# Kernel tuning notes

Hardware: AMD Instinct MI355X
Metric: run time of the kernel (lower is better)

The kernel has to match this reference:

```python
import jax, jax.numpy as jnp
import numpy as np

N_NODES = 50000


def _sage_layer(x, edges, W_neigh, W_self, b):
    """HeteroGraphConv(sum) of per-relation DGL SAGEConv(mean).

    x:        [N, F_in] node features (single node type)
    edges:    [R, 2, E] int (src, dst) per relation
    W_neigh:  [R, F_in, F_out], W_self: [R, F_in, F_out], b: [R, F_out]
    returns:  [N, F_out]
    """
    N = x.shape[0]
    R = edges.shape[0]
    out = jnp.zeros((N, W_neigh.shape[-1]), dtype=x.dtype)
    for r in range(R):  # small fixed number of relation types
        src = edges[r, 0]
        dst = edges[r, 1]
        # mean-aggregate neighbor features onto dst
        s = jax.ops.segment_sum(x[src], dst, num_segments=N)          # [N, F_in]
        deg = jax.ops.segment_sum(jnp.ones_like(dst, dtype=x.dtype), dst,
                                  num_segments=N)                     # [N]
        mean = s / jnp.maximum(deg, 1.0)[:, None]                     # zero-deg -> 0
        # SAGEConv(mean): fc_self(h_dst) + fc_neigh(mean_neigh) + bias
        out = out + x @ W_self[r] + mean @ W_neigh[r] + b[r]
    return out


def setup_inputs() -> dict:
    key = jax.random.key(0)
    ks = jax.random.split(key, 10)
    F_in, H, O, R, E = 128, 128, 64, 2, 800000
    scale_in = 1.0 / np.sqrt(F_in)
    scale_h = 1.0 / np.sqrt(H)
    return {
        "x": jax.random.normal(ks[0], (N_NODES, F_in), dtype=jnp.float32),
        "edges": jax.random.randint(ks[1], (R, 2, E), 0, N_NODES, dtype=jnp.int32),
        "neg_edges": jax.random.randint(ks[2], (2, E), 0, N_NODES, dtype=jnp.int32),
        "W_neigh1": jax.random.normal(ks[3], (R, F_in, H), jnp.float32) * scale_in,
        "W_self1": jax.random.normal(ks[4], (R, F_in, H), jnp.float32) * scale_in,
        "b1": jnp.zeros((R, H), jnp.float32),
        "W_neigh2": jax.random.normal(ks[5], (R, H, O), jnp.float32) * scale_h,
        "W_self2": jax.random.normal(ks[6], (R, H, O), jnp.float32) * scale_h,
        "b2": jnp.zeros((R, O), jnp.float32),
    }


def reference(x, edges, neg_edges, W_neigh1, W_self1, b1, W_neigh2, W_self2, b2):
    h = _sage_layer(x, edges, W_neigh1, W_self1, b1)
    h = jax.nn.relu(h)
    h = _sage_layer(h, edges, W_neigh2, W_self2, b2)          # [N, O]
    # HeteroDotProductPredictor: u_dot_v on edges of the scored etype (rel 0)
    pos_score = jnp.sum(h[edges[0, 0]] * h[edges[0, 1]], axis=-1)      # [E]
    neg_score = jnp.sum(h[neg_edges[0]] * h[neg_edges[1]], axis=-1)    # [E_neg]
    return pos_score, neg_score
```

## Files before the change

kernel.cpp:

```cpp
#include <hip/hip_runtime.h>


#define BW 128
#define NBK_MAX 1024
#define EPB 8192

typedef __attribute__((ext_vector_type(8))) short bf16x8;
typedef __attribute__((ext_vector_type(4))) float floatx4;
typedef __attribute__((ext_vector_type(2))) float floatx2;

__device__ __forceinline__ unsigned short f2bf(float f) {
    unsigned u = __float_as_uint(f);
    unsigned r = u + 0x7FFFu + ((u >> 16) & 1u);
    return (unsigned short)(r >> 16);
}
__device__ __forceinline__ unsigned pack2(float a, float b) {
    return (unsigned)f2bf(a) | ((unsigned)f2bf(b) << 16);
}
__device__ __forceinline__ float bflo(unsigned v) { return __uint_as_float(v << 16); }
__device__ __forceinline__ float bfhi(unsigned v) { return __uint_as_float(v & 0xFFFF0000u); }
#define RFL(x) __builtin_amdgcn_readfirstlane(x)

#if defined(__has_builtin) && __has_builtin(__builtin_amdgcn_cvt_pk_f32_fp8)
__device__ __forceinline__ floatx2 fp8lo(unsigned v) {
    return __builtin_amdgcn_cvt_pk_f32_fp8((int)v, false);
}
__device__ __forceinline__ floatx2 fp8hi(unsigned v) {
    return __builtin_amdgcn_cvt_pk_f32_fp8((int)v, true);
}
#else
__device__ __forceinline__ float fp8_1(unsigned b) {
    return __uint_as_float(((b & 0x80u) << 24) | ((b & 0x7Fu) << 20)) * 0x1.0p+120f;
}
__device__ __forceinline__ floatx2 fp8lo(unsigned v) {
    floatx2 r; r.x = fp8_1(v & 0xFFu); r.y = fp8_1((v >> 8) & 0xFFu); return r;
}
__device__ __forceinline__ floatx2 fp8hi(unsigned v) {
    floatx2 r; r.x = fp8_1((v >> 16) & 0xFFu); r.y = fp8_1((v >> 24) & 0xFFu); return r;
}
#endif

#if defined(__has_builtin) && __has_builtin(__builtin_amdgcn_cvt_pk_fp8_f32)
__device__ __forceinline__ unsigned f32x4_fp8x4(float a, float b, float c, float d) {
    unsigned lo = __builtin_amdgcn_cvt_pk_fp8_f32(a, b, 0, false);
    return __builtin_amdgcn_cvt_pk_fp8_f32(c, d, lo, true);
}
#else
__device__ __forceinline__ unsigned f2fp8(float x) {
    float m = fminf(fabsf(x), 448.0f);
    unsigned u = __float_as_uint(m * 0x1.0p-120f);
    unsigned r = (u + 0x7FFFFu + ((u >> 20) & 1u)) >> 20;
    if (r > 0x7Eu) r = 0x7Eu;
    return r | ((__float_as_uint(x) >> 24) & 0x80u);
}
__device__ __forceinline__ unsigned f32x4_fp8x4(float a, float b, float c, float d) {
    return f2fp8(a) | (f2fp8(b) << 8) | (f2fp8(c) << 16) | (f2fp8(d) << 24);
}
#endif

__global__ __launch_bounds__(256) void
bucket_count_kernel(const int* __restrict__ edges, int* __restrict__ bcnt,
                    int NBK, int E)
{
    __shared__ int cnt[2 * NBK_MAX];
    const int rbT = 2 * NBK;
    const int t = threadIdx.x;
    for (int k = t; k < rbT; k += 256) cnt[k] = 0;
    __syncthreads();
    long long start = (long long)blockIdx.x * EPB;
    long long twoE = 2LL * E;
    for (int u = 0; u < EPB / 256; ++u) {
        long long idx = start + u * 256 + t;
        if (idx < twoE) {
            int r = idx >= E;
            int e = (int)(idx - (long long)r * E);
            int d = edges[(size_t)r * 2 * E + E + e];
            atomicAdd(&cnt[r * NBK + (d >> 7)], 1);
        }
    }
    __syncthreads();
    for (int k = t; k < rbT; k += 256)
        if (cnt[k]) atomicAdd(&bcnt[k], cnt[k]);
}

__global__ __launch_bounds__(1024) void
bucket_scan_kernel(const int* __restrict__ bcnt, int* __restrict__ bko,
                   int rbT, int twoE)
{
    __shared__ int sm[1024];
    int t = threadIdx.x;
    int v = (t < rbT) ? bcnt[t] : 0;
    sm[t] = v;
    __syncthreads();
    for (int s = 1; s < 1024; s <<= 1) {
        int u = (t >= s) ? sm[t - s] : 0;
        __syncthreads();
        sm[t] += u;
        __syncthreads();
    }
    if (t < rbT) bko[t] = sm[t] - v;
    if (t == 0) bko[rbT] = twoE;
}

__global__ __launch_bounds__(256) void
partition_kernel(const int* __restrict__ edges, const int* __restrict__ bko,
                 int* __restrict__ gcur, uint2* __restrict__ staging,
                 int NBK, int E)
{
    __shared__ int cnt[2 * NBK_MAX];
    __shared__ int base[2 * NBK_MAX];
    const int rbT = 2 * NBK;
    const int t = threadIdx.x;
    for (int k = t; k < rbT; k += 256) cnt[k] = 0;
    __syncthreads();
    long long start = (long long)blockIdx.x * EPB;
    long long twoE = 2LL * E;
    for (int u = 0; u < EPB / 256; ++u) {
        long long idx = start + u * 256 + t;
        if (idx < twoE) {
            int r = idx >= E;
            int e = (int)(idx - (long long)r * E);
            int d = edges[(size_t)r * 2 * E + E + e];
            atomicAdd(&cnt[r * NBK + (d >> 7)], 1);
        }
    }
    __syncthreads();
    for (int k = t; k < rbT; k += 256) {
        int c0 = cnt[k];
        if (c0) base[k] = bko[k] + atomicAdd(&gcur[k], c0);
        cnt[k] = 0;
    }
    __syncthreads();
    for (int u = 0; u < EPB / 256; ++u) {
        long long idx = start + u * 256 + t;
        if (idx < twoE) {
            int r = idx >= E;
            int e = (int)(idx - (long long)r * E);
            int s = edges[(size_t)r * 2 * E + e];
            int d = edges[(size_t)r * 2 * E + E + e];
            int rb = r * NBK + (d >> 7);
            int pos = atomicAdd(&cnt[rb], 1);
            staging[(size_t)base[rb] + pos] = make_uint2((unsigned)s, (unsigned)d);
        }
    }
}

__global__ __launch_bounds__(256) void
bucket_csr_kernel(const uint2* __restrict__ staging, const int* __restrict__ bko,
                  int* __restrict__ csr, int* __restrict__ off,
                  int NBK, int N)
{
    __shared__ int hist[BW], excl[BW], cur[BW], sc[BW];
    const int rb = blockIdx.x;
    const int r = rb / NBK;
    const int b = rb % NBK;
    const int node0 = b * BW;
    const int nn = min(BW, N - node0);
    const int cbase = bko[rb];
    const int c = bko[rb + 1] - cbase;
    const int t = threadIdx.x;

    if (t < BW) { hist[t] = 0; cur[t] = 0; }
    __syncthreads();
    for (int k = t; k < c; k += 256)
        atomicAdd(&hist[(int)staging[(size_t)cbase + k].y - node0], 1);
    __syncthreads();
    if (t < BW) sc[t] = hist[t];
    __syncthreads();
    for (int s = 1; s < BW; s <<= 1) {
        int v = (t < BW && t >= s) ? sc[t - s] : 0;
        __syncthreads();
        if (t < BW) sc[t] += v;
        __syncthreads();
    }
    if (t < BW) excl[t] = sc[t] - hist[t];
    if (t < nn) off[(size_t)r * N + node0 + t] = cbase + excl[t];
    __syncthreads();
    for (int k = t; k < c; k += 256) {
        uint2 pr = staging[(size_t)cbase + k];
        int l = (int)pr.y - node0;
        int pos = atomicAdd(&cur[l], 1);
        csr[(size_t)cbase + excl[l] + pos] = (int)pr.x;
    }
}

__global__ void cvt_kernel(const float* __restrict__ in,
                           unsigned short* __restrict__ o,
                           unsigned char* __restrict__ o8, int n4)
{
    int t = blockIdx.x * blockDim.x + threadIdx.x;
    if (t >= n4) return;
    float4 v = ((const float4*)in)[t];
    ushort4 r;
    r.x = f2bf(v.x); r.y = f2bf(v.y); r.z = f2bf(v.z); r.w = f2bf(v.w);
    ((ushort4*)o)[t] = r;
    ((unsigned*)o8)[t] = f32x4_fp8x4(v.x, v.y, v.z, v.w);
}

__global__ void prep_kernel(const float* __restrict__ Ws1, const float* __restrict__ Wn1,
                            const float* __restrict__ b1,
                            const float* __restrict__ Ws2, const float* __restrict__ Wn2,
                            const float* __restrict__ b2,
                            unsigned short* __restrict__ WT1z, unsigned short* __restrict__ WT1a,
                            unsigned short* __restrict__ WT1b, float* __restrict__ bc1,
                            unsigned short* __restrict__ WT2z, unsigned short* __restrict__ WT2a,
                            unsigned short* __restrict__ WT2b, float* __restrict__ bc2)
{
    int t = blockIdx.x * blockDim.x + threadIdx.x;
    if (t < 16384) {
        int n = t >> 7, k = t & 127;
        int in = k * 128 + n;
        WT1z[t] = f2bf(Ws1[in] + Ws1[16384 + in]);
        WT1a[t] = f2bf(Wn1[in]);
        WT1b[t] = f2bf(Wn1[16384 + in]);
    }
    if (t < 8192) {
        int n = t >> 7, k = t & 127;
        int in = k * 64 + n;
        WT2z[t] = f2bf(Ws2[in] + Ws2[8192 + in]);
        WT2a[t] = f2bf(Wn2[in]);
        WT2b[t] = f2bf(Wn2[8192 + in]);
    }
    if (t < 128) bc1[t] = b1[t] + b1[128 + t];
    if (t < 64)  bc2[t] = b2[t] + b2[64 + t];
}

__global__ __launch_bounds__(256) void
agg1_kernel(const unsigned char* __restrict__ xb8,
            const int* __restrict__ csr, const int* __restrict__ off,
            unsigned short* __restrict__ m0, unsigned short* __restrict__ m1,
            int N, int twoE)
{
    int w = blockIdx.x * 4 + (threadIdx.x >> 6);
    int lane = threadIdx.x & 63;
    if (w >= N) return;
    const int col = lane * 2;
    const unsigned char* xc = xb8 + col;

    float sx0 = 0.f, sy0 = 0.f, sx1 = 0.f, sy1 = 0.f;

    int o0 = RFL(off[w]);
    int o1 = RFL(off[w + 1]);
    int d0 = o1 - o0;
    int j = o0;
    for (; j + 7 < o1; j += 8) {
        int s0 = RFL(csr[j]);     int s1 = RFL(csr[j + 1]);
        int s2 = RFL(csr[j + 2]); int s3 = RFL(csr[j + 3]);
        int s4 = RFL(csr[j + 4]); int s5 = RFL(csr[j + 5]);
        int s6 = RFL(csr[j + 6]); int s7 = RFL(csr[j + 7]);
        unsigned a0 = *(const unsigned short*)(xc + (size_t)s0 * 128);
        unsigned a1 = *(const unsigned short*)(xc + (size_t)s1 * 128);
        unsigned a2 = *(const unsigned short*)(xc + (size_t)s2 * 128);
        unsigned a3 = *(const unsigned short*)(xc + (size_t)s3 * 128);
        unsigned a4 = *(const unsigned short*)(xc + (size_t)s4 * 128);
        unsigned a5 = *(const unsigned short*)(xc + (size_t)s5 * 128);
        unsigned a6 = *(const unsigned short*)(xc + (size_t)s6 * 128);
        unsigned a7 = *(const unsigned short*)(xc + (size_t)s7 * 128);
        floatx2 v0 = fp8lo(a0); floatx2 v1 = fp8lo(a1);
        floatx2 v2 = fp8lo(a2); floatx2 v3 = fp8lo(a3);
        floatx2 v4 = fp8lo(a4); floatx2 v5 = fp8lo(a5);
        floatx2 v6 = fp8lo(a6); floatx2 v7 = fp8lo(a7);
        sx0 += ((v0.x + v1.x) + (v2.x + v3.x)) + ((v4.x + v5.x) + (v6.x + v7.x));
        sy0 += ((v0.y + v1.y) + (v2.y + v3.y)) + ((v4.y + v5.y) + (v6.y + v7.y));
    }
    for (; j < o1; ++j) {
        int s0 = RFL(csr[j]);
        floatx2 v = fp8lo(*(const unsigned short*)(xc + (size_t)s0 * 128));
        sx0 += v.x; sy0 += v.y;
    }

    int p = N + w;
    o0 = RFL(off[p]);
    o1 = (p + 1 < 2 * N) ? RFL(off[p + 1]) : twoE;
    int d1 = o1 - o0;
    j = o0;
    for (; j + 7 < o1; j += 8) {
        int s0 = RFL(csr[j]);     int s1 = RFL(csr[j + 1]);
        int s2 = RFL(csr[j + 2]); int s3 = RFL(csr[j + 3]);
        int s4 = RFL(csr[j + 4]); int s5 = RFL(csr[j + 5]);
        int s6 = RFL(csr[j + 6]); int s7 = RFL(csr[j + 7]);
        unsigned a0 = *(const unsigned short*)(xc + (size_t)s0 * 128);
        unsigned a1 = *(const unsigned short*)(xc + (size_t)s1 * 128);
        unsigned a2 = *(const unsigned short*)(xc + (size_t)s2 * 128);
        unsigned a3 = *(const unsigned short*)(xc + (size_t)s3 * 128);
        unsigned a4 = *(const unsigned short*)(xc + (size_t)s4 * 128);
        unsigned a5 = *(const unsigned short*)(xc + (size_t)s5 * 128);
        unsigned a6 = *(const unsigned short*)(xc + (size_t)s6 * 128);
        unsigned a7 = *(const unsigned short*)(xc + (size_t)s7 * 128);
        floatx2 v0 = fp8lo(a0); floatx2 v1 = fp8lo(a1);
        floatx2 v2 = fp8lo(a2); floatx2 v3 = fp8lo(a3);
        floatx2 v4 = fp8lo(a4); floatx2 v5 = fp8lo(a5);
        floatx2 v6 = fp8lo(a6); floatx2 v7 = fp8lo(a7);
        sx1 += ((v0.x + v1.x) + (v2.x + v3.x)) + ((v4.x + v5.x) + (v6.x + v7.x));
        sy1 += ((v0.y + v1.y) + (v2.y + v3.y)) + ((v4.y + v5.y) + (v6.y + v7.y));
    }
    for (; j < o1; ++j) {
        int s0 = RFL(csr[j]);
        floatx2 v = fp8lo(*(const unsigned short*)(xc + (size_t)s0 * 128));
        sx1 += v.x; sy1 += v.y;
    }

    float inv0 = 1.0f / fmaxf((float)d0, 1.0f);
    float inv1 = 1.0f / fmaxf((float)d1, 1.0f);
    *(unsigned*)(m0 + (size_t)w * 128 + col) = pack2(sx0 * inv0, sy0 * inv0);
    *(unsigned*)(m1 + (size_t)w * 128 + col) = pack2(sx1 * inv1, sy1 * inv1);
}

__global__ __launch_bounds__(256) void
gemm1_fused_kernel(const unsigned short* __restrict__ xb,
                   const unsigned short* __restrict__ m0,
                   const unsigned short* __restrict__ m1,
                   const unsigned short* __restrict__ WTz,
                   const unsigned short* __restrict__ WTa,
                   const unsigned short* __restrict__ WTb,
                   const float* __restrict__ bias,
                   unsigned short* __restrict__ h1b, int N)
{
    __shared__ float eb[64][129];

    const int tid = threadIdx.x;
    const int wave = tid >> 6;
    const int lane = tid & 63;
    const int m = lane & 15;
    const int quad = lane >> 4;

    floatx4 acc[8];
    const floatx4 z4 = {0.f, 0.f, 0.f, 0.f};
#pragma unroll
    for (int t = 0; t < 8; ++t) acc[t] = z4;

    int arow = blockIdx.x * 64 + wave * 16 + m;
    if (arow >= N) arow = N - 1;
    const size_t abase = (size_t)arow * 128 + quad * 8;

#pragma unroll
    for (int s = 0; s < 4; ++s) {
        bf16x8 ax = *(const bf16x8*)(xb + abase + s * 32);
        bf16x8 a0 = *(const bf16x8*)(m0 + abase + s * 32);
        bf16x8 a1 = *(const bf16x8*)(m1 + abase + s * 32);
#pragma unroll
        for (int t = 0; t < 8; ++t) {
            const size_t bo = (size_t)(t * 16 + m) * 128 + s * 32 + quad * 8;
            acc[t] = __builtin_amdgcn_mfma_f32_16x16x32_bf16(
                ax, *(const bf16x8*)(WTz + bo), acc[t], 0, 0, 0);
            acc[t] = __builtin_amdgcn_mfma_f32_16x16x32_bf16(
                a0, *(const bf16x8*)(WTa + bo), acc[t], 0, 0, 0);
            acc[t] = __builtin_amdgcn_mfma_f32_16x16x32_bf16(
                a1, *(const bf16x8*)(WTb + bo), acc[t], 0, 0, 0);
        }
    }

#pragma unroll
    for (int t = 0; t < 8; ++t)
#pragma unroll
        for (int i = 0; i < 4; ++i)
            eb[wave * 16 + quad * 4 + i][t * 16 + m] = acc[t][i];
    __syncthreads();

#pragma unroll
    for (int j = 0; j < 4; ++j) {
        int lr = wave * 16 + j * 4 + quad;
        int grow = blockIdx.x * 64 + lr;
        if (grow < N) {
#pragma unroll
            for (int i = 0; i < 2; ++i) {
                int c0 = (i * 16 + m) * 4;
                float v0 = fmaxf(eb[lr][c0 + 0] + bias[c0 + 0], 0.0f);
                float v1 = fmaxf(eb[lr][c0 + 1] + bias[c0 + 1], 0.0f);
                float v2 = fmaxf(eb[lr][c0 + 2] + bias[c0 + 2], 0.0f);
                float v3 = fmaxf(eb[lr][c0 + 3] + bias[c0 + 3], 0.0f);
                ushort4 u;
                u.x = f2bf(v0); u.y = f2bf(v1); u.z = f2bf(v2); u.w = f2bf(v3);
                *(ushort4*)(h1b + (size_t)grow * 128 + c0) = u;
            }
        }
    }
}

__global__ __launch_bounds__(256) void
gemm2_fused_kernel(const unsigned short* __restrict__ Ab,
                   const unsigned short* __restrict__ WTz,
                   const unsigned short* __restrict__ WTa,
                   const unsigned short* __restrict__ WTb,
                   const float* __restrict__ bias,
                   float* __restrict__ zf,
                   unsigned char* __restrict__ t08, unsigned char* __restrict__ t18,
                   int N)
{
    __shared__ float eb[64][65];

    const int tid = threadIdx.x;
    const int wave = tid >> 6;
    const int lane = tid & 63;
    const int m = lane & 15;
    const int quad = lane >> 4;

    floatx4 accz[4], acca[4], accb[4];
    const floatx4 z4 = {0.f, 0.f, 0.f, 0.f};
#pragma unroll
    for (int t = 0; t < 4; ++t) { accz[t] = z4; acca[t] = z4; accb[t] = z4; }

    int arow = blockIdx.x * 64 + wave * 16 + m;
    if (arow >= N) arow = N - 1;
    const unsigned short* aptr = Ab + (size_t)arow * 128 + quad * 8;

#pragma unroll
    for (int s = 0; s < 4; ++s) {
        bf16x8 a = *(const bf16x8*)(aptr + s * 32);
#pragma unroll
        for (int t = 0; t < 4; ++t) {
            const size_t bo = (size_t)(t * 16 + m) * 128 + s * 32 + quad * 8;
            accz[t] = __builtin_amdgcn_mfma_f32_16x16x32_bf16(
                a, *(const bf16x8*)(WTz + bo), accz[t], 0, 0, 0);
            acca[t] = __builtin_amdgcn_mfma_f32_16x16x32_bf16(
                a, *(const bf16x8*)(WTa + bo), acca[t], 0, 0, 0);
            accb[t] = __builtin_amdgcn_mfma_f32_16x16x32_bf16(
                a, *(const bf16x8*)(WTb + bo), accb[t], 0, 0, 0);
        }
    }

#pragma unroll
    for (int t = 0; t < 4; ++t)
#pragma unroll
        for (int i = 0; i < 4; ++i)
            eb[wave * 16 + quad * 4 + i][t * 16 + m] = accz[t][i];
    __syncthreads();
#pragma unroll
    for (int j = 0; j < 4; ++j) {
        int lr = wave * 16 + j * 4 + quad;
        int gr = blockIdx.x * 64 + lr;
        if (gr < N) {
            int c0 = m * 4;
            float4 o;
            o.x = eb[lr][c0 + 0] + bias[c0 + 0];
            o.y = eb[lr][c0 + 1] + bias[c0 + 1];
            o.z = eb[lr][c0 + 2] + bias[c0 + 2];
            o.w = eb[lr][c0 + 3] + bias[c0 + 3];
            *(float4*)(zf + (size_t)gr * 64 + c0) = o;
        }
    }
    __syncthreads();

#pragma unroll
    for (int t = 0; t < 4; ++t)
#pragma unroll
        for (int i = 0; i < 4; ++i)
            eb[wave * 16 + quad * 4 + i][t * 16 + m] = acca[t][i];
    __syncthreads();
#pragma unroll
    for (int j = 0; j < 4; ++j) {
        int lr = wave * 16 + j * 4 + quad;
        int gr = blockIdx.x * 64 + lr;
        if (gr < N) {
            int c0 = m * 4;
            *(unsigned*)(t08 + (size_t)gr * 64 + c0) = f32x4_fp8x4(
                eb[lr][c0 + 0], eb[lr][c0 + 1], eb[lr][c0 + 2], eb[lr][c0 + 3]);
        }
    }
    __syncthreads();

#pragma unroll
    for (int t = 0; t < 4; ++t)
#pragma unroll
        for (int i = 0; i < 4; ++i)
            eb[wave * 16 + quad * 4 + i][t * 16 + m] = accb[t][i];
    __syncthreads();
#pragma unroll
    for (int j = 0; j < 4; ++j) {
        int lr = wave * 16 + j * 4 + quad;
        int gr = blockIdx.x * 64 + lr;
        if (gr < N) {
            int c0 = m * 4;
            *(unsigned*)(t18 + (size_t)gr * 64 + c0) = f32x4_fp8x4(
                eb[lr][c0 + 0], eb[lr][c0 + 1], eb[lr][c0 + 2], eb[lr][c0 + 3]);
        }
    }
}

__global__ __launch_bounds__(256) void
agg2_kernel(const unsigned char* __restrict__ t08,
            const unsigned char* __restrict__ t18,
            const float* __restrict__ z2,
            const int* __restrict__ csr, const int* __restrict__ off,
            unsigned short* __restrict__ h2b, int N, int twoE)
{
    int w = blockIdx.x * 4 + (threadIdx.x >> 6);
    int lane = threadIdx.x & 63;
    if (w >= N) return;
    const int q = lane >> 4;
    const int col = (lane & 15) * 4;
    const unsigned char* t0c = t08 + col;
    const unsigned char* t1c = t18 + col;

    float a0 = 0.f, a1 = 0.f, a2 = 0.f, a3 = 0.f;
    float b0 = 0.f, b1 = 0.f, b2 = 0.f, b3 = 0.f;

    int o0 = RFL(off[w]);
    int o1 = RFL(off[w + 1]);
    int d0 = o1 - o0;
    int j = o0;
    for (; j + 15 < o1; j += 16) {
        int r0 = csr[j + q];
        int r1 = csr[j + 4 + q];
        int r2 = csr[j + 8 + q];
        int r3 = csr[j + 12 + q];
        unsigned v0 = *(const unsigned*)(t0c + (size_t)r0 * 64);
        unsigned v1 = *(const unsigned*)(t0c + (size_t)r1 * 64);
        unsigned v2 = *(const unsigned*)(t0c + (size_t)r2 * 64);
        unsigned v3 = *(const unsigned*)(t0c + (size_t)r3 * 64);
        floatx2 l0 = fp8lo(v0), h0 = fp8hi(v0);
        floatx2 l1 = fp8lo(v1), h1 = fp8hi(v1);
        floatx2 l2 = fp8lo(v2), h2 = fp8hi(v2);
        floatx2 l3 = fp8lo(v3), h3 = fp8hi(v3);
        a0 += (l0.x + l1.x) + (l2.x + l3.x);
        a1 += (l0.y + l1.y) + (l2.y + l3.y);
        a2 += (h0.x + h1.x) + (h2.x + h3.x);
        a3 += (h0.y + h1.y) + (h2.y + h3.y);
    }
    for (; j + 3 < o1; j += 4) {
        int r = csr[j + q];
        unsigned v = *(const unsigned*)(t0c + (size_t)r * 64);
        floatx2 l = fp8lo(v), h = fp8hi(v);
        a0 += l.x; a1 += l.y; a2 += h.x; a3 += h.y;
    }
    if (j < o1 && q < o1 - j) {
        int r = csr[j + q];
        unsigned v = *(const unsigned*)(t0c + (size_t)r * 64);
        floatx2 l = fp8lo(v), h = fp8hi(v);
        a0 += l.x; a1 += l.y; a2 += h.x; a3 += h.y;
    }

    int p = N + w;
    o0 = RFL(off[p]);
    o1 = (p + 1 < 2 * N) ? RFL(off[p + 1]) : twoE;
    int d1 = o1 - o0;
    j = o0;
    for (; j + 15 < o1; j += 16) {
        int r0 = csr[j + q];
        int r1 = csr[j + 4 + q];
        int r2 = csr[j + 8 + q];
        int r3 = csr[j + 12 + q];
        unsigned v0 = *(const unsigned*)(t1c + (size_t)r0 * 64);
        unsigned v1 = *(const unsigned*)(t1c + (size_t)r1 * 64);
        unsigned v2 = *(const unsigned*)(t1c + (size_t)r2 * 64);
        unsigned v3 = *(const unsigned*)(t1c + (size_t)r3 * 64);
        floatx2 l0 = fp8lo(v0), h0 = fp8hi(v0);
        floatx2 l1 = fp8lo(v1), h1 = fp8hi(v1);
        floatx2 l2 = fp8lo(v2), h2 = fp8hi(v2);
        floatx2 l3 = fp8lo(v3), h3 = fp8hi(v3);
        b0 += (l0.x + l1.x) + (l2.x + l3.x);
        b1 += (l0.y + l1.y) + (l2.y + l3.y);
        b2 += (h0.x + h1.x) + (h2.x + h3.x);
        b3 += (h0.y + h1.y) + (h2.y + h3.y);
    }
    for (; j + 3 < o1; j += 4) {
        int r = csr[j + q];
        unsigned v = *(const unsigned*)(t1c + (size_t)r * 64);
        floatx2 l = fp8lo(v), h = fp8hi(v);
        b0 += l.x; b1 += l.y; b2 += h.x; b3 += h.y;
    }
    if (j < o1 && q < o1 - j) {
        int r = csr[j + q];
        unsigned v = *(const unsigned*)(t1c + (size_t)r * 64);
        floatx2 l = fp8lo(v), h = fp8hi(v);
        b0 += l.x; b1 += l.y; b2 += h.x; b3 += h.y;
    }

    a0 += __shfl_xor(a0, 16); a1 += __shfl_xor(a1, 16);
    a2 += __shfl_xor(a2, 16); a3 += __shfl_xor(a3, 16);
    b0 += __shfl_xor(b0, 16); b1 += __shfl_xor(b1, 16);
    b2 += __shfl_xor(b2, 16); b3 += __shfl_xor(b3, 16);
    a0 += __shfl_xor(a0, 32); a1 += __shfl_xor(a1, 32);
    a2 += __shfl_xor(a2, 32); a3 += __shfl_xor(a3, 32);
    b0 += __shfl_xor(b0, 32); b1 += __shfl_xor(b1, 32);
    b2 += __shfl_xor(b2, 32); b3 += __shfl_xor(b3, 32);
    if (q == 0) {
        float inv0 = 1.0f / fmaxf((float)d0, 1.0f);
        float inv1 = 1.0f / fmaxf((float)d1, 1.0f);
        float4 z = *(const float4*)(z2 + (size_t)w * 64 + col);
        float h0v = z.x + a0 * inv0 + b0 * inv1;
        float h1v = z.y + a1 * inv0 + b1 * inv1;
        float h2v = z.z + a2 * inv0 + b2 * inv1;
        float h3v = z.w + a3 * inv0 + b3 * inv1;
        uint2 u;
        u.x = pack2(h0v, h1v);
        u.y = pack2(h2v, h3v);
        *(uint2*)(h2b + (size_t)w * 64 + col) = u;
    }
}

__global__ __launch_bounds__(256) void
score_kernel(const unsigned short* __restrict__ h,
             const int* __restrict__ edges, const int* __restrict__ neg,
             float* __restrict__ out, int E, int En)
{
    int t = blockIdx.x * blockDim.x + threadIdx.x;
    int e = t >> 3;
    int c = t & 7;
    if (e >= E + En) return;
    int sI, dI, oI;
    if (e < E) { sI = edges[e]; dI = edges[E + e]; oI = e; }
    else { int en = e - E; sI = neg[en]; dI = neg[En + en]; oI = E + en; }
    uint4 va = *(const uint4*)(h + (size_t)sI * 64 + c * 8);
    uint4 vb = *(const uint4*)(h + (size_t)dI * 64 + c * 8);
    float s = 0.0f;
    s = fmaf(bflo(va.x), bflo(vb.x), s);
    s = fmaf(bfhi(va.x), bfhi(vb.x), s);
    s = fmaf(bflo(va.y), bflo(vb.y), s);
    s = fmaf(bfhi(va.y), bfhi(vb.y), s);
    s = fmaf(bflo(va.z), bflo(vb.z), s);
    s = fmaf(bfhi(va.z), bfhi(vb.z), s);
    s = fmaf(bflo(va.w), bflo(vb.w), s);
    s = fmaf(bfhi(va.w), bfhi(vb.w), s);
    s += __shfl_xor(s, 1);
    s += __shfl_xor(s, 2);
    s += __shfl_xor(s, 4);
    if (c == 0) out[oI] = s;
}

extern "C" void kernel_launch(void* const* d_in, const int* in_sizes, int n_in,
                              void* d_out, int out_size, void* d_ws, size_t ws_size,
                              hipStream_t stream)
{
    const float* x     = (const float*)d_in[0];
    const int*   edges = (const int*)d_in[1];
    const int*   neg   = (const int*)d_in[2];
    const float* Wn1   = (const float*)d_in[3];
    const float* Ws1   = (const float*)d_in[4];
    const float* b1    = (const float*)d_in[5];
    const float* Wn2   = (const float*)d_in[6];
    const float* Ws2   = (const float*)d_in[7];
    const float* b2    = (const float*)d_in[8];
    float* out = (float*)d_out;

    const int Fin = 128, R = 2;
    const int N  = in_sizes[0] / Fin;
    const int E  = in_sizes[1] / (R * 2);
    const int En = in_sizes[2] / 2;
    const int twoE = 2 * E;
    const int NBK = (N + BW - 1) / BW;
    const int rbT = 2 * NBK;

    const size_t nb128 = (size_t)N * 128 * sizeof(unsigned short);
    char* p = (char*)d_ws;

    uint2* staging       = (uint2*)p;
    unsigned char* xb8   = (unsigned char*)p;
    float* z2            = (float*)p;
    {
        size_t r0 = (size_t)twoE * sizeof(uint2);
        size_t r1 = (size_t)N * 64 * sizeof(float);
        size_t r2 = (size_t)N * 128;
        size_t rm = r0 > r1 ? r0 : r1;
        if (r2 > rm) rm = r2;
        p += rm;
    }
    unsigned short* m0  = (unsigned short*)p; p += nb128;
    unsigned short* m1  = (unsigned short*)p; p += nb128;
    unsigned short* xb  = (unsigned short*)p; p += nb128;
    unsigned short* h1b = (unsigned short*)p; p += nb128;
    unsigned short* WT1z = (unsigned short*)p; p += 16384 * 2;
    unsigned short* WT1a = (unsigned short*)p; p += 16384 * 2;
    unsigned short* WT1b = (unsigned short*)p; p += 16384 * 2;
    unsigned short* WT2z = (unsigned short*)p; p += 8192 * 2;
    unsigned short* WT2a = (unsigned short*)p; p += 8192 * 2;
    unsigned short* WT2b = (unsigned short*)p; p += 8192 * 2;
    float* bc1 = (float*)p; p += 128 * sizeof(float);
    float* bc2 = (float*)p; p += 64 * sizeof(float);
    int* bcnt = (int*)p; p += (size_t)2 * NBK_MAX * sizeof(int);
    int* gcur = (int*)p; p += (size_t)2 * NBK_MAX * sizeof(int);
    int* bko  = (int*)p; p += ((size_t)2 * NBK_MAX + 1) * sizeof(int);
    int* off  = (int*)p; p += (size_t)2 * N * sizeof(int);
    int* csr  = (int*)p;

    unsigned char*  t08 = (unsigned char*)m0;
    unsigned char*  t18 = t08 + (size_t)N * 64;
    unsigned short* h2b = m1;

    const int BS = 256;
    const int edge_blocks = (twoE + EPB - 1) / EPB;
    const int gx = (N + 63) / 64;

    hipMemsetAsync(bcnt, 0, (size_t)4 * NBK_MAX * sizeof(int), stream);
    bucket_count_kernel<<<edge_blocks, BS, 0, stream>>>(edges, bcnt, NBK, E);
    bucket_scan_kernel<<<1, 1024, 0, stream>>>(bcnt, bko, rbT, twoE);
    partition_kernel<<<edge_blocks, BS, 0, stream>>>(edges, bko, gcur, staging, NBK, E);
    bucket_csr_kernel<<<rbT, BS, 0, stream>>>(staging, bko, csr, off, NBK, N);

    cvt_kernel<<<(N * 32 + BS - 1) / BS, BS, 0, stream>>>(x, xb, xb8, N * 32);
    prep_kernel<<<(16384 + BS - 1) / BS, BS, 0, stream>>>(
        Ws1, Wn1, b1, Ws2, Wn2, b2,
        WT1z, WT1a, WT1b, bc1, WT2z, WT2a, WT2b, bc2);

    agg1_kernel<<<(N + 3) / 4, BS, 0, stream>>>(xb8, csr, off, m0, m1, N, twoE);
    gemm1_fused_kernel<<<gx, BS, 0, stream>>>(xb, m0, m1, WT1z, WT1a, WT1b,
                                              bc1, h1b, N);

    gemm2_fused_kernel<<<gx, BS, 0, stream>>>(h1b, WT2z, WT2a, WT2b, bc2,
                                              z2, t08, t18, N);
    agg2_kernel<<<(N + 3) / 4, BS, 0, stream>>>(t08, t18, z2, csr, off, h2b, N, twoE);

    score_kernel<<<((E + En) * 8 + BS - 1) / BS, BS, 0, stream>>>(
        h2b, edges, neg, out, E, En);
}
```

Measured before the change: 363.8 us.

## Split gemm1 columns across grid y and drop LDS epilogue staging

gemm1 now launches a 2D grid where each block computes 64 of the 128 output columns, which halves accumulator registers and doubles block count. Both gemm kernels preload all A fragments up front and write results straight from MFMA accumulators instead of staging through shared memory with barriers. The direct stores are scalar and strided: 2-byte bf16, 4-byte float and 1-byte fp8 per lane at row stride. This can hurt write coalescing compared with the previous vectorized row writes. A, m0 and m1 are also reloaded by both column halves in gemm1.

```diff
diff --git a/kernel.cpp b/kernel.cpp
--- a/kernel.cpp
+++ b/kernel.cpp
@@ -44,6 +44,9 @@
 __device__ __forceinline__ unsigned f32x4_fp8x4(float a, float b, float c, float d) {
     unsigned lo = __builtin_amdgcn_cvt_pk_fp8_f32(a, b, 0, false);
     return __builtin_amdgcn_cvt_pk_fp8_f32(c, d, lo, true);
+}
+__device__ __forceinline__ unsigned char f2fp8_1(float x) {
+    return (unsigned char)(__builtin_amdgcn_cvt_pk_fp8_f32(x, x, 0, false) & 0xFFu);
 }
 #else
 __device__ __forceinline__ unsigned f2fp8(float x) {
@@ -55,6 +58,9 @@
 }
 __device__ __forceinline__ unsigned f32x4_fp8x4(float a, float b, float c, float d) {
     return f2fp8(a) | (f2fp8(b) << 8) | (f2fp8(c) << 16) | (f2fp8(d) << 24);
+}
+__device__ __forceinline__ unsigned char f2fp8_1(float x) {
+    return (unsigned char)f2fp8(x);
 }
 #endif
 
@@ -316,63 +322,74 @@
                    const float* __restrict__ bias,
                    unsigned short* __restrict__ h1b, int N)
 {
-    __shared__ float eb[64][129];
-
     const int tid = threadIdx.x;
     const int wave = tid >> 6;
     const int lane = tid & 63;
     const int m = lane & 15;
     const int quad = lane >> 4;
-
-    floatx4 acc[8];
+    const int colbase = blockIdx.y * 64;
+
+    floatx4 acc[4];
     const floatx4 z4 = {0.f, 0.f, 0.f, 0.f};
 #pragma unroll
-    for (int t = 0; t < 8; ++t) acc[t] = z4;
+    for (int t = 0; t < 4; ++t) acc[t] = z4;
 
     int arow = blockIdx.x * 64 + wave * 16 + m;
     if (arow >= N) arow = N - 1;
-    const size_t abase = (size_t)arow * 128 + quad * 8;
+    const size_t ab = (size_t)arow * 128 + quad * 8;
+
+    bf16x8 ax0 = *(const bf16x8*)(xb + ab);
+    bf16x8 ax1 = *(const bf16x8*)(xb + ab + 32);
+    bf16x8 ax2 = *(const bf16x8*)(xb + ab + 64);
+    bf16x8 ax3 = *(const bf16x8*)(xb + ab + 96);
+    bf16x8 a00 = *(const bf16x8*)(m0 + ab);
+    bf16x8 a01 = *(const bf16x8*)(m0 + ab + 32);
+    bf16x8 a02 = *(const bf16x8*)(m0 + ab + 64);
+    bf16x8 a03 = *(const bf16x8*)(m0 + ab + 96);
+    bf16x8 a10 = *(const bf16x8*)(m1 + ab);
+    bf16x8 a11 = *(const bf16x8*)(m1 + ab + 32);
+    bf16x8 a12 = *(const bf16x8*)(m1 + ab + 64);
+    bf16x8 a13 = *(const bf16x8*)(m1 + ab + 96);
 
 #pragma unroll
-    for (int s = 0; s < 4; ++s) {
-        bf16x8 ax = *(const bf16x8*)(xb + abase + s * 32);
-        bf16x8 a0 = *(const bf16x8*)(m0 + abase + s * 32);
-        bf16x8 a1 = *(const bf16x8*)(m1 + abase + s * 32);
+    for (int t = 0; t < 4; ++t) {
+        const size_t bo = (size_t)(colbase + t * 16 + m) * 128 + quad * 8;
+        acc[t] = __builtin_amdgcn_mfma_f32_16x16x32_bf16(
+            ax0, *(const bf16x8*)(WTz + bo), acc[t], 0, 0, 0);
+        acc[t] = __builtin_amdgcn_mfma_f32_16x16x32_bf16(
+            a00, *(const bf16x8*)(WTa + bo), acc[t], 0, 0, 0);
+        acc[t] = __builtin_amdgcn_mfma_f32_16x16x32_bf16(
+            a10, *(const bf16x8*)(WTb + bo), acc[t], 0, 0, 0);
+        acc[t] = __builtin_amdgcn_mfma_f32_16x16x32_bf16(
+            ax1, *(const bf16x8*)(WTz + bo + 32), acc[t], 0, 0, 0);
+        acc[t] = __builtin_amdgcn_mfma_f32_16x16x32_bf16(
+            a01, *(const bf16x8*)(WTa + bo + 32), acc[t], 0, 0, 0);
+        acc[t] = __builtin_amdgcn_mfma_f32_16x16x32_bf16(
+            a11, *(const bf16x8*)(WTb + bo + 32), acc[t], 0, 0, 0);
+        acc[t] = __builtin_amdgcn_mfma_f32_16x16x32_bf16(
+            ax2, *(const bf16x8*)(WTz + bo + 64), acc[t], 0, 0, 0);
+        acc[t] = __builtin_amdgcn_mfma_f32_16x16x32_bf16(
+            a02, *(const bf16x8*)(WTa + bo + 64), acc[t], 0, 0, 0);
+        acc[t] = __builtin_amdgcn_mfma_f32_16x16x32_bf16(
+            a12, *(const bf16x8*)(WTb + bo + 64), acc[t], 0, 0, 0);
+        acc[t] = __builtin_amdgcn_mfma_f32_16x16x32_bf16(
+            ax3, *(const bf16x8*)(WTz + bo + 96), acc[t], 0, 0, 0);
+        acc[t] = __builtin_amdgcn_mfma_f32_16x16x32_bf16(
+            a03, *(const bf16x8*)(WTa + bo + 96), acc[t], 0, 0, 0);
+        acc[t] = __builtin_amdgcn_mfma_f32_16x16x32_bf16(
+            a13, *(const bf16x8*)(WTb + bo + 96), acc[t], 0, 0, 0);
+    }
+
+    const int gr0 = blockIdx.x * 64 + wave * 16 + quad * 4;
 #pragma unroll
-        for (int t = 0; t < 8; ++t) {
-            const size_t bo = (size_t)(t * 16 + m) * 128 + s * 32 + quad * 8;
-            acc[t] = __builtin_amdgcn_mfma_f32_16x16x32_bf16(
-                ax, *(const bf16x8*)(WTz + bo), acc[t], 0, 0, 0);
-            acc[t] = __builtin_amdgcn_mfma_f32_16x16x32_bf16(
-                a0, *(const bf16x8*)(WTa + bo), acc[t], 0, 0, 0);
-            acc[t] = __builtin_amdgcn_mfma_f32_16x16x32_bf16(
-                a1, *(const bf16x8*)(WTb + bo), acc[t], 0, 0, 0);
-        }
-    }
-
+    for (int t = 0; t < 4; ++t) {
+        int colg = colbase + t * 16 + m;
+        float bv = bias[colg];
 #pragma unroll
-    for (int t = 0; t < 8; ++t)
-#pragma unroll
-        for (int i = 0; i < 4; ++i)
-            eb[wave * 16 + quad * 4 + i][t * 16 + m] = acc[t][i];
-    __syncthreads();
-
-#pragma unroll
-    for (int j = 0; j < 4; ++j) {
-        int lr = wave * 16 + j * 4 + quad;
-        int grow = blockIdx.x * 64 + lr;
-        if (grow < N) {
-#pragma unroll
-            for (int i = 0; i < 2; ++i) {
-                int c0 = (i * 16 + m) * 4;
-                float v0 = fmaxf(eb[lr][c0 + 0] + bias[c0 + 0], 0.0f);
-                float v1 = fmaxf(eb[lr][c0 + 1] + bias[c0 + 1], 0.0f);
-                float v2 = fmaxf(eb[lr][c0 + 2] + bias[c0 + 2], 0.0f);
-                float v3 = fmaxf(eb[lr][c0 + 3] + bias[c0 + 3], 0.0f);
-                ushort4 u;
-                u.x = f2bf(v0); u.y = f2bf(v1); u.z = f2bf(v2); u.w = f2bf(v3);
-                *(ushort4*)(h1b + (size_t)grow * 128 + c0) = u;
-            }
+        for (int i = 0; i < 4; ++i) {
+            int gr = gr0 + i;
+            if (gr < N)
+                h1b[(size_t)gr * 128 + colg] = f2bf(fmaxf(acc[t][i] + bv, 0.0f));
         }
     }
 }
@@ -387,8 +404,6 @@
                    unsigned char* __restrict__ t08, unsigned char* __restrict__ t18,
                    int N)
 {
-    __shared__ float eb[64][65];
-
     const int tid = threadIdx.x;
     const int wave = tid >> 6;
     const int lane = tid & 63;
@@ -402,77 +417,55 @@
 
     int arow = blockIdx.x * 64 + wave * 16 + m;
     if (arow >= N) arow = N - 1;
-    const unsigned short* aptr = Ab + (size_t)arow * 128 + quad * 8;
+    const size_t ab = (size_t)arow * 128 + quad * 8;
+
+    bf16x8 h0 = *(const bf16x8*)(Ab + ab);
+    bf16x8 h1 = *(const bf16x8*)(Ab + ab + 32);
+    bf16x8 h2 = *(const bf16x8*)(Ab + ab + 64);
+    bf16x8 h3 = *(const bf16x8*)(Ab + ab + 96);
 
 #pragma unroll
-    for (int s = 0; s < 4; ++s) {
-        bf16x8 a = *(const bf16x8*)(aptr + s * 32);
+    for (int t = 0; t < 4; ++t) {
+        const size_t bo = (size_t)(t * 16 + m) * 128 + quad * 8;
+        accz[t] = __builtin_amdgcn_mfma_f32_16x16x32_bf16(
+            h0, *(const bf16x8*)(WTz + bo), accz[t], 0, 0, 0);
+        acca[t] = __builtin_amdgcn_mfma_f32_16x16x32_bf16(
+            h0, *(const bf16x8*)(WTa + bo), acca[t], 0, 0, 0);
+        accb[t] = __builtin_amdgcn_mfma_f32_16x16x32_bf16(
+            h0, *(const bf16x8*)(WTb + bo), accb[t], 0, 0, 0);
+        accz[t] = __builtin_amdgcn_mfma_f32_16x16x32_bf16(
+            h1, *(const bf16x8*)(WTz + bo + 32), accz[t], 0, 0, 0);
+        acca[t] = __builtin_amdgcn_mfma_f32_16x16x32_bf16(
+            h1, *(const bf16x8*)(WTa + bo + 32), acca[t], 0, 0, 0);
+        accb[t] = __builtin_amdgcn_mfma_f32_16x16x32_bf16(
+            h1, *(const bf16x8*)(WTb + bo + 32), accb[t], 0, 0, 0);
+        accz[t] = __builtin_amdgcn_mfma_f32_16x16x32_bf16(
+            h2, *(const bf16x8*)(WTz + bo + 64), accz[t], 0, 0, 0);
+        acca[t] = __builtin_amdgcn_mfma_f32_16x16x32_bf16(
+            h2, *(const bf16x8*)(WTa + bo + 64), acca[t], 0, 0, 0);
+        accb[t] = __builtin_amdgcn_mfma_f32_16x16x32_bf16(
+            h2, *(const bf16x8*)(WTb + bo + 64), accb[t], 0, 0, 0);
+        accz[t] = __builtin_amdgcn_mfma_f32_16x16x32_bf16(
+            h3, *(const bf16x8*)(WTz + bo + 96), accz[t], 0, 0, 0);
+        acca[t] = __builtin_amdgcn_mfma_f32_16x16x32_bf16(
+            h3, *(const bf16x8*)(WTa + bo + 96), acca[t], 0, 0, 0);
+        accb[t] = __builtin_amdgcn_mfma_f32_16x16x32_bf16(
+            h3, *(const bf16x8*)(WTb + bo + 96), accb[t], 0, 0, 0);
+    }
+
+    const int gr0 = blockIdx.x * 64 + wave * 16 + quad * 4;
 #pragma unroll
-        for (int t = 0; t < 4; ++t) {
-            const size_t bo = (size_t)(t * 16 + m) * 128 + s * 32 + quad * 8;
-            accz[t] = __builtin_amdgcn_mfma_f32_16x16x32_bf16(
-                a, *(const bf16x8*)(WTz + bo), accz[t], 0, 0, 0);
-            acca[t] = __builtin_amdgcn_mfma_f32_16x16x32_bf16(
-                a, *(const bf16x8*)(WTa + bo), acca[t], 0, 0, 0);
-            accb[t] = __builtin_amdgcn_mfma_f32_16x16x32_bf16(
-                a, *(const bf16x8*)(WTb + bo), accb[t], 0, 0, 0);
-        }
-    }
-
+    for (int t = 0; t < 4; ++t) {
+        int colg = t * 16 + m;
+        float bv = bias[colg];
 #pragma unroll
-    for (int t = 0; t < 4; ++t)
-#pragma unroll
-        for (int i = 0; i < 4; ++i)
-            eb[wave * 16 + quad * 4 + i][t * 16 + m] = accz[t][i];
-    __syncthreads();
-#pragma unroll
-    for (int j = 0; j < 4; ++j) {
-        int lr = wave * 16 + j * 4 + quad;
-        int gr = blockIdx.x * 64 + lr;
-        if (gr < N) {
-            int c0 = m * 4;
-            float4 o;
-            o.x = eb[lr][c0 + 0] + bias[c0 + 0];
-            o.y = eb[lr][c0 + 1] + bias[c0 + 1];
-            o.z = eb[lr][c0 + 2] + bias[c0 + 2];
-            o.w = eb[lr][c0 + 3] + bias[c0 + 3];
-            *(float4*)(zf + (size_t)gr * 64 + c0) = o;
-        }
-    }
-    __syncthreads();
-
-#pragma unroll
-    for (int t = 0; t < 4; ++t)
-#pragma unroll
-        for (int i = 0; i < 4; ++i)
-            eb[wave * 16 + quad * 4 + i][t * 16 + m] = acca[t][i];
-    __syncthreads();
-#pragma unroll
-    for (int j = 0; j < 4; ++j) {
-        int lr = wave * 16 + j * 4 + quad;
-        int gr = blockIdx.x * 64 + lr;
-        if (gr < N) {
-            int c0 = m * 4;
-            *(unsigned*)(t08 + (size_t)gr * 64 + c0) = f32x4_fp8x4(
-                eb[lr][c0 + 0], eb[lr][c0 + 1], eb[lr][c0 + 2], eb[lr][c0 + 3]);
-        }
-    }
-    __syncthreads();
-
-#pragma unroll
-    for (int t = 0; t < 4; ++t)
-#pragma unroll
-        for (int i = 0; i < 4; ++i)
-            eb[wave * 16 + quad * 4 + i][t * 16 + m] = accb[t][i];
-    __syncthreads();
-#pragma unroll
-    for (int j = 0; j < 4; ++j) {
-        int lr = wave * 16 + j * 4 + quad;
-        int gr = blockIdx.x * 64 + lr;
-        if (gr < N) {
-            int c0 = m * 4;
-            *(unsigned*)(t18 + (size_t)gr * 64 + c0) = f32x4_fp8x4(
-                eb[lr][c0 + 0], eb[lr][c0 + 1], eb[lr][c0 + 2], eb[lr][c0 + 3]);
+        for (int i = 0; i < 4; ++i) {
+            int gr = gr0 + i;
+            if (gr < N) {
+                zf[(size_t)gr * 64 + colg] = accz[t][i] + bv;
+                t08[(size_t)gr * 64 + colg] = f2fp8_1(acca[t][i]);
+                t18[(size_t)gr * 64 + colg] = f2fp8_1(accb[t][i]);
+            }
         }
     }
 }
@@ -693,8 +686,11 @@
         WT1z, WT1a, WT1b, bc1, WT2z, WT2a, WT2b, bc2);
 
     agg1_kernel<<<(N + 3) / 4, BS, 0, stream>>>(xb8, csr, off, m0, m1, N, twoE);
-    gemm1_fused_kernel<<<gx, BS, 0, stream>>>(xb, m0, m1, WT1z, WT1a, WT1b,
-                                              bc1, h1b, N);
+    {
+        dim3 g(gx, 2);
+        gemm1_fused_kernel<<<g, BS, 0, stream>>>(xb, m0, m1, WT1z, WT1a, WT1b,
+                                                 bc1, h1b, N);
+    }
 
     gemm2_fused_kernel<<<gx, BS, 0, stream>>>(h1b, WT2z, WT2a, WT2b, bc2,
                                               z2, t08, t18, N);
```

Measured after the change: 363.6 us. No clear change (-0.1%).
